# Kernel optimization log

Hardware: AMD Instinct MI355X
Metric: run time of the kernel (lower is better)

The kernel has to match this reference:

```python
import jax, jax.numpy as jnp
import numpy as np

B, C, H, W = 16, 96, 64, 64
N = H * W
BN = B * N
K = 16  # neighbors per node
E = BN * K
C_OUT = 96


def setup_inputs() -> dict:
    key = jax.random.key(0)
    k1, k2, k3, k4 = jax.random.split(key, 4)
    x = jax.random.normal(k1, (B, C, H, W), dtype=jnp.float32)
    # KNN-style edge list over flat node ids (node = b*N + n):
    # every node appears K times as a target (row 0), random sources (row 1).
    dst = jnp.repeat(jnp.arange(BN, dtype=jnp.int64), K)
    src = jax.random.randint(k2, (E,), 0, BN, dtype=jnp.int64)
    edge_index = jnp.stack([dst, src], axis=0)
    Wc = jax.random.normal(k3, (C_OUT, 2 * C), dtype=jnp.float32) * 0.05
    bc = jax.random.normal(k4, (C_OUT,), dtype=jnp.float32) * 0.05
    return {"x": x, "edge_index": edge_index, "Wc": Wc, "bc": bc}


def reference(x, edge_index, Wc, bc):
    b, c, h, w = x.shape
    n = h * w
    # Flatten to node features [B*N, C] with node id = b*N + n
    feats = x.reshape(b, c, n).transpose(0, 2, 1).reshape(b * n, c)
    # Max-relative aggregation: gather, subtract, scatter-max over targets
    diff = feats[edge_index[1]] - feats[edge_index[0]]        # [E, C]
    agg = jax.ops.segment_max(diff, edge_index[0], num_segments=b * n)  # [BN, C]
    x_j = agg.reshape(b, n, c).transpose(0, 2, 1)             # [B, C, N]
    x_n = x.reshape(b, c, n)                                   # [B, C, N]
    # Interleaved channel concat: (x_0, xj_0, x_1, xj_1, ...) -> [B, 2C, N]
    cat = jnp.stack([x_n, x_j], axis=2).reshape(b, 2 * c, n)
    # BasicConv: 1x1 conv (GEMM over channels) + bias + ReLU
    out = jnp.einsum('oc,bcn->bon', Wc, cat) + bc[None, :, None]
    out = jax.nn.relu(out)
    return out.reshape(b, -1, h, w)
```

## Files before the change

### kernel.cpp

```cpp
#include <hip/hip_runtime.h>

#define B_   16
#define C_   96
#define N_   4096
#define BN_  65536
#define K_   16
#define E_   (BN_ * K_)

typedef __attribute__((ext_vector_type(8))) short bf16x8;
typedef __attribute__((ext_vector_type(4))) float f32x4;

union FragU { uint32_t u[4]; bf16x8 v; };

__device__ __forceinline__ uint32_t pack2_bf16(float a, float b) {
    uint32_t ua = __builtin_bit_cast(uint32_t, a);
    uint32_t ub = __builtin_bit_cast(uint32_t, b);
    ua = (ua + 0x7fffu + ((ua >> 16) & 1u)) >> 16;
    ub = (ub + 0x7fffu + ((ub >> 16) & 1u)) >> 16;
    return (ua & 0xffffu) | (ub << 16);
}
__device__ __forceinline__ float lo16f(uint32_t u) {
    return __builtin_bit_cast(float, u << 16);
}
__device__ __forceinline__ float hi16f(uint32_t u) {
    return __builtin_bit_cast(float, u & 0xffff0000u);
}

__global__ __launch_bounds__(256) void transpose_k(const float* __restrict__ x,
                                                   ushort* __restrict__ feats_bf) {
    __shared__ float tile[32][65];
    int b  = blockIdx.z;
    int c0 = blockIdx.y * 32;
    int n0 = blockIdx.x * 64;
    const float* xp = x + (size_t)b * C_ * N_;
    for (int t = threadIdx.x; t < 32 * 64; t += 256) {
        int c = t >> 6, n = t & 63;
        tile[c][n] = xp[(size_t)(c0 + c) * N_ + n0 + n];
    }
    __syncthreads();
    ushort* fp = feats_bf + ((size_t)b * N_ + n0) * C_ + c0;
    for (int t = threadIdx.x; t < 64 * 16; t += 256) {
        int n = t >> 4, cq = t & 15;
        uint32_t p = pack2_bf16(tile[2 * cq][n], tile[2 * cq + 1][n]);
        *(uint32_t*)(fp + (size_t)n * C_ + 2 * cq) = p;
    }
}

__global__ __launch_bounds__(256) void gather_max_k(const ushort* __restrict__ feats,
                                                    const int* __restrict__ src,
                                                    ushort* __restrict__ agg_bf,
                                                    const float* __restrict__ Wc,
                                                    ushort* __restrict__ Wp) {
    int tid = threadIdx.x;
    if (blockIdx.x >= 2048) {
        int t = (blockIdx.x - 2048) * 256 + tid;
        if (t >= 36 * 64) return;
        int fid = t >> 6, l = t & 63;
        int ks = fid / 6, to = fid % 6;
        int o = to * 16 + (l & 15), g = l >> 4;
        uint32_t packed[4];
#pragma unroll
        for (int h = 0; h < 4; h++) {
            int e0 = 2 * h, e1 = 2 * h + 1;
            int k0 = ks * 32 + 4 * g + (e0 & 3) + 16 * (e0 >> 2);
            int k1 = ks * 32 + 4 * g + (e1 & 3) + 16 * (e1 >> 2);
            int ko0 = (k0 < 96) ? 2 * k0 : 2 * (k0 - 96) + 1;
            int ko1 = (k1 < 96) ? 2 * k1 : 2 * (k1 - 96) + 1;
            packed[h] = pack2_bf16(Wc[(size_t)o * 192 + ko0],
                                   Wc[(size_t)o * 192 + ko1]);
        }
        ((uint4*)Wp)[t] = make_uint4(packed[0], packed[1], packed[2], packed[3]);
        return;
    }

    int ln  = tid >> 3;
    int r   = tid & 7;
    size_t i = (size_t)blockIdx.x * 32 + ln;
    const int* s = src + i * K_;

    float m[12];
#pragma unroll
    for (int j = 0; j < 12; j++) m[j] = -3.0e38f;

#pragma unroll
    for (int q = 0; q < 4; q++) {
        int4 iv = ((const int4*)s)[q];
        int ids[4] = {iv.x, iv.y, iv.z, iv.w};
#pragma unroll
        for (int kk = 0; kk < 4; kk++) {
            const uint2* row = (const uint2*)(feats + (size_t)ids[kk] * C_);
#pragma unroll
            for (int j = 0; j < 3; j++) {
                uint2 v = row[r + 8 * j];
                m[4 * j + 0] = fmaxf(m[4 * j + 0], lo16f(v.x));
                m[4 * j + 1] = fmaxf(m[4 * j + 1], hi16f(v.x));
                m[4 * j + 2] = fmaxf(m[4 * j + 2], lo16f(v.y));
                m[4 * j + 3] = fmaxf(m[4 * j + 3], hi16f(v.y));
            }
        }
    }

    const uint2* own = (const uint2*)(feats + i * (size_t)C_);
    ushort* ap = agg_bf + i * (size_t)C_;
#pragma unroll
    for (int j = 0; j < 3; j++) {
        uint2 o = own[r + 8 * j];
        uint2 p;
        p.x = pack2_bf16(m[4 * j + 0] - lo16f(o.x), m[4 * j + 1] - hi16f(o.x));
        p.y = pack2_bf16(m[4 * j + 2] - lo16f(o.y), m[4 * j + 3] - hi16f(o.y));
        *(uint2*)(ap + (size_t)(r + 8 * j) * 4) = p;
    }
}

__global__ __launch_bounds__(512) void conv_mfma_k(const ushort* __restrict__ feats_bf,
                                                   const ushort* __restrict__ agg_bf,
                                                   const ushort* __restrict__ Wp,
                                                   const float* __restrict__ bc,
                                                   float* __restrict__ out) {
    __shared__ ushort A_lds[128 * 200];
    int tid = threadIdx.x;
    int w = tid >> 6, l = tid & 63;
    int blk = blockIdx.x;
    int b = blk >> 5;
    int n0 = (blk & 31) << 7;

    float bcr[6];
#pragma unroll
    for (int to = 0; to < 6; to++) bcr[to] = bc[to * 16 + (l & 15)];

    const ushort* fb = feats_bf + ((size_t)b * N_ + n0) * C_;
    const ushort* ab = agg_bf + ((size_t)b * N_ + n0) * C_;
#pragma unroll
    for (int i = 0; i < 6; i++) {
        int tau = i * 512 + tid;
        int n = tau / 24;
        int p = tau - n * 24;
        const ushort* srcp = (p < 12) ? (fb + (size_t)n * C_ + 8 * p)
                                      : (ab + (size_t)n * C_ + 8 * (p - 12));
        uint4 u = *(const uint4*)srcp;
        if (n & 1) { uint32_t t0 = u.x, t1 = u.y; u.x = u.z; u.y = u.w; u.z = t0; u.w = t1; }
        int slot = p ^ ((n >> 1) & 7);
        *(uint4*)&A_lds[n * 200 + slot * 8] = u;
    }
    __syncthreads();

    f32x4 acc[6];
#pragma unroll
    for (int to = 0; to < 6; to++) acc[to] = (f32x4){0.f, 0.f, 0.f, 0.f};

    const uint4* wp4 = (const uint4*)Wp;
    int g = l >> 4;
    int m = (l & 15) << 2;
    int nrow = w * 16 + (l & 15);
    int abase = nrow * 200;

#pragma unroll
    for (int ks = 0; ks < 6; ks++) {
        FragU bfrag[6];
#pragma unroll
        for (int to = 0; to < 6; to++) {
            uint4 u = wp4[(ks * 6 + to) * 64 + l];
            bfrag[to].u[0] = u.x; bfrag[to].u[1] = u.y;
            bfrag[to].u[2] = u.z; bfrag[to].u[3] = u.w;
        }
        int k1 = ks * 32 + 4 * g;
        uint2 lo = *(const uint2*)&A_lds[abase + (k1 ^ m)];
        uint2 hi = *(const uint2*)&A_lds[abase + ((k1 + 16) ^ m)];
        FragU afrag;
        afrag.u[0] = lo.x; afrag.u[1] = lo.y;
        afrag.u[2] = hi.x; afrag.u[3] = hi.y;
#pragma unroll
        for (int to = 0; to < 6; to++)
            acc[to] = __builtin_amdgcn_mfma_f32_16x16x32_bf16(
                afrag.v, bfrag[to].v, acc[to], 0, 0, 0);
    }

    int nl = n0 + w * 16 + ((l >> 4) << 2);
#pragma unroll
    for (int to = 0; to < 6; to++) {
        int o = to * 16 + (l & 15);
        float4 v;
        v.x = fmaxf(acc[to][0] + bcr[to], 0.0f);
        v.y = fmaxf(acc[to][1] + bcr[to], 0.0f);
        v.z = fmaxf(acc[to][2] + bcr[to], 0.0f);
        v.w = fmaxf(acc[to][3] + bcr[to], 0.0f);
        *(float4*)(out + ((size_t)b * C_ + o) * N_ + nl) = v;
    }
}

extern "C" void kernel_launch(void* const* d_in, const int* in_sizes, int n_in,
                              void* d_out, int out_size, void* d_ws, size_t ws_size,
                              hipStream_t stream) {
    const float* x   = (const float*)d_in[0];
    const int*   ei  = (const int*)d_in[1];
    const float* Wc  = (const float*)d_in[2];
    const float* bc  = (const float*)d_in[3];
    float* out = (float*)d_out;

    const int* src = ei + E_;

    ushort* feats_bf = (ushort*)d_ws;
    ushort* agg_bf   = (ushort*)((char*)d_ws + (size_t)BN_ * C_ * 2);
    ushort* Wp       = (ushort*)((char*)d_ws + (size_t)BN_ * C_ * 4);

    dim3 gA(N_ / 64, C_ / 32, B_);
    transpose_k<<<gA, 256, 0, stream>>>(x, feats_bf);

    gather_max_k<<<2057, 256, 0, stream>>>(feats_bf, src, agg_bf, Wc, Wp);

    conv_mfma_k<<<B_ * (N_ / 128), 512, 0, stream>>>(feats_bf, agg_bf, Wp, bc, out);
}
```

Before: 57.01 us.

## Fuse gather-max aggregation into conv kernel and weight packing into transpose

Moves the neighbor gather/max-relative aggregation into the MFMA conv kernel, which writes the aggregated bf16 features straight into the shared-memory A tile instead of round-tripping them through a global agg buffer. Weight packing moves into the transpose kernel, cutting the pipeline from three launches to two. This removes the global write and re-read of agg and one launch, but the conv kernel now has only 512 blocks doing latency-bound random gathers (two nodes per thread), so less parallelism is available to hide gather latency.

```diff
diff --git a/kernel.cpp b/kernel.cpp
--- a/kernel.cpp
+++ b/kernel.cpp
@@ -26,34 +26,13 @@
     return __builtin_bit_cast(float, u & 0xffff0000u);
 }
 
-__global__ __launch_bounds__(256) void transpose_k(const float* __restrict__ x,
-                                                   ushort* __restrict__ feats_bf) {
-    __shared__ float tile[32][65];
-    int b  = blockIdx.z;
-    int c0 = blockIdx.y * 32;
-    int n0 = blockIdx.x * 64;
-    const float* xp = x + (size_t)b * C_ * N_;
-    for (int t = threadIdx.x; t < 32 * 64; t += 256) {
-        int c = t >> 6, n = t & 63;
-        tile[c][n] = xp[(size_t)(c0 + c) * N_ + n0 + n];
-    }
-    __syncthreads();
-    ushort* fp = feats_bf + ((size_t)b * N_ + n0) * C_ + c0;
-    for (int t = threadIdx.x; t < 64 * 16; t += 256) {
-        int n = t >> 4, cq = t & 15;
-        uint32_t p = pack2_bf16(tile[2 * cq][n], tile[2 * cq + 1][n]);
-        *(uint32_t*)(fp + (size_t)n * C_ + 2 * cq) = p;
-    }
-}
-
-__global__ __launch_bounds__(256) void gather_max_k(const ushort* __restrict__ feats,
-                                                    const int* __restrict__ src,
-                                                    ushort* __restrict__ agg_bf,
-                                                    const float* __restrict__ Wc,
-                                                    ushort* __restrict__ Wp) {
-    int tid = threadIdx.x;
-    if (blockIdx.x >= 2048) {
-        int t = (blockIdx.x - 2048) * 256 + tid;
+__global__ __launch_bounds__(256) void transpose_pack_k(const float* __restrict__ x,
+                                                        ushort* __restrict__ feats_bf,
+                                                        const float* __restrict__ Wc,
+                                                        ushort* __restrict__ Wp) {
+    int blk = blockIdx.x;
+    if (blk >= 3072) {
+        int t = (blk - 3072) * 256 + threadIdx.x;
         if (t >= 36 * 64) return;
         int fid = t >> 6, l = t & 63;
         int ks = fid / 6, to = fid % 6;
@@ -72,51 +51,30 @@
         ((uint4*)Wp)[t] = make_uint4(packed[0], packed[1], packed[2], packed[3]);
         return;
     }
-
-    int ln  = tid >> 3;
-    int r   = tid & 7;
-    size_t i = (size_t)blockIdx.x * 32 + ln;
-    const int* s = src + i * K_;
-
-    float m[12];
-#pragma unroll
-    for (int j = 0; j < 12; j++) m[j] = -3.0e38f;
-
-#pragma unroll
-    for (int q = 0; q < 4; q++) {
-        int4 iv = ((const int4*)s)[q];
-        int ids[4] = {iv.x, iv.y, iv.z, iv.w};
-#pragma unroll
-        for (int kk = 0; kk < 4; kk++) {
-            const uint2* row = (const uint2*)(feats + (size_t)ids[kk] * C_);
-#pragma unroll
-            for (int j = 0; j < 3; j++) {
-                uint2 v = row[r + 8 * j];
-                m[4 * j + 0] = fmaxf(m[4 * j + 0], lo16f(v.x));
-                m[4 * j + 1] = fmaxf(m[4 * j + 1], hi16f(v.x));
-                m[4 * j + 2] = fmaxf(m[4 * j + 2], lo16f(v.y));
-                m[4 * j + 3] = fmaxf(m[4 * j + 3], hi16f(v.y));
-            }
-        }
-    }
-
-    const uint2* own = (const uint2*)(feats + i * (size_t)C_);
-    ushort* ap = agg_bf + i * (size_t)C_;
-#pragma unroll
-    for (int j = 0; j < 3; j++) {
-        uint2 o = own[r + 8 * j];
-        uint2 p;
-        p.x = pack2_bf16(m[4 * j + 0] - lo16f(o.x), m[4 * j + 1] - hi16f(o.x));
-        p.y = pack2_bf16(m[4 * j + 2] - lo16f(o.y), m[4 * j + 3] - hi16f(o.y));
-        *(uint2*)(ap + (size_t)(r + 8 * j) * 4) = p;
-    }
-}
-
-__global__ __launch_bounds__(512) void conv_mfma_k(const ushort* __restrict__ feats_bf,
-                                                   const ushort* __restrict__ agg_bf,
-                                                   const ushort* __restrict__ Wp,
-                                                   const float* __restrict__ bc,
-                                                   float* __restrict__ out) {
+    __shared__ float tile[32][65];
+    int b   = blk / 192;
+    int rem = blk - b * 192;
+    int c0  = (rem >> 6) * 32;
+    int n0  = (rem & 63) * 64;
+    const float* xp = x + (size_t)b * C_ * N_;
+    for (int t = threadIdx.x; t < 32 * 64; t += 256) {
+        int c = t >> 6, n = t & 63;
+        tile[c][n] = xp[(size_t)(c0 + c) * N_ + n0 + n];
+    }
+    __syncthreads();
+    ushort* fp = feats_bf + ((size_t)b * N_ + n0) * C_ + c0;
+    for (int t = threadIdx.x; t < 64 * 16; t += 256) {
+        int n = t >> 4, cq = t & 15;
+        uint32_t p = pack2_bf16(tile[2 * cq][n], tile[2 * cq + 1][n]);
+        *(uint32_t*)(fp + (size_t)n * C_ + 2 * cq) = p;
+    }
+}
+
+__global__ __launch_bounds__(512) void gconv_k(const ushort* __restrict__ feats,
+                                               const int* __restrict__ src,
+                                               const ushort* __restrict__ Wp,
+                                               const float* __restrict__ bc,
+                                               float* __restrict__ out) {
     __shared__ ushort A_lds[128 * 200];
     int tid = threadIdx.x;
     int w = tid >> 6, l = tid & 63;
@@ -124,25 +82,64 @@
     int b = blk >> 5;
     int n0 = (blk & 31) << 7;
 
-    float bcr[6];
-#pragma unroll
-    for (int to = 0; to < 6; to++) bcr[to] = bc[to * 16 + (l & 15)];
-
-    const ushort* fb = feats_bf + ((size_t)b * N_ + n0) * C_;
-    const ushort* ab = agg_bf + ((size_t)b * N_ + n0) * C_;
-#pragma unroll
-    for (int i = 0; i < 6; i++) {
+    const ushort* fb = feats + ((size_t)b * N_ + n0) * C_;
+#pragma unroll
+    for (int i = 0; i < 3; i++) {
         int tau = i * 512 + tid;
-        int n = tau / 24;
-        int p = tau - n * 24;
-        const ushort* srcp = (p < 12) ? (fb + (size_t)n * C_ + 8 * p)
-                                      : (ab + (size_t)n * C_ + 8 * (p - 12));
-        uint4 u = *(const uint4*)srcp;
+        int n = tau / 12;
+        int p = tau - n * 12;
+        uint4 u = *(const uint4*)(fb + (size_t)n * C_ + 8 * p);
         if (n & 1) { uint32_t t0 = u.x, t1 = u.y; u.x = u.z; u.y = u.w; u.z = t0; u.w = t1; }
         int slot = p ^ ((n >> 1) & 7);
         *(uint4*)&A_lds[n * 200 + slot * 8] = u;
     }
+
+#pragma unroll
+    for (int s = 0; s < 2; s++) {
+        int ln = s * 64 + (tid >> 3);
+        int r  = tid & 7;
+        size_t i = (size_t)b * N_ + n0 + ln;
+        const int* sp = src + i * K_;
+
+        float m[12];
+#pragma unroll
+        for (int j = 0; j < 12; j++) m[j] = -3.0e38f;
+
+#pragma unroll
+        for (int q = 0; q < 4; q++) {
+            int4 iv = ((const int4*)sp)[q];
+            int ids[4] = {iv.x, iv.y, iv.z, iv.w};
+#pragma unroll
+            for (int kk = 0; kk < 4; kk++) {
+                const uint2* row = (const uint2*)(feats + (size_t)ids[kk] * C_);
+#pragma unroll
+                for (int j = 0; j < 3; j++) {
+                    uint2 v = row[r + 8 * j];
+                    m[4 * j + 0] = fmaxf(m[4 * j + 0], lo16f(v.x));
+                    m[4 * j + 1] = fmaxf(m[4 * j + 1], hi16f(v.x));
+                    m[4 * j + 2] = fmaxf(m[4 * j + 2], lo16f(v.y));
+                    m[4 * j + 3] = fmaxf(m[4 * j + 3], hi16f(v.y));
+                }
+            }
+        }
+
+        const uint2* own = (const uint2*)(feats + i * (size_t)C_);
+#pragma unroll
+        for (int j = 0; j < 3; j++) {
+            uint2 o = own[r + 8 * j];
+            uint2 p;
+            p.x = pack2_bf16(m[4 * j + 0] - lo16f(o.x), m[4 * j + 1] - hi16f(o.x));
+            p.y = pack2_bf16(m[4 * j + 2] - lo16f(o.y), m[4 * j + 3] - hi16f(o.y));
+            int qa = r + 8 * j;
+            int idx = ln * 200 + ((96 + 4 * qa) ^ ((ln & 15) << 2));
+            *(uint2*)&A_lds[idx] = p;
+        }
+    }
     __syncthreads();
+
+    float bcr[6];
+#pragma unroll
+    for (int to = 0; to < 6; to++) bcr[to] = bc[to * 16 + (l & 15)];
 
     f32x4 acc[6];
 #pragma unroll
@@ -150,9 +147,8 @@
 
     const uint4* wp4 = (const uint4*)Wp;
     int g = l >> 4;
-    int m = (l & 15) << 2;
-    int nrow = w * 16 + (l & 15);
-    int abase = nrow * 200;
+    int msk = (l & 15) << 2;
+    int abase = (w * 16 + (l & 15)) * 200;
 
 #pragma unroll
     for (int ks = 0; ks < 6; ks++) {
@@ -164,8 +160,8 @@
             bfrag[to].u[2] = u.z; bfrag[to].u[3] = u.w;
         }
         int k1 = ks * 32 + 4 * g;
-        uint2 lo = *(const uint2*)&A_lds[abase + (k1 ^ m)];
-        uint2 hi = *(const uint2*)&A_lds[abase + ((k1 + 16) ^ m)];
+        uint2 lo = *(const uint2*)&A_lds[abase + (k1 ^ msk)];
+        uint2 hi = *(const uint2*)&A_lds[abase + ((k1 + 16) ^ msk)];
         FragU afrag;
         afrag.u[0] = lo.x; afrag.u[1] = lo.y;
         afrag.u[2] = hi.x; afrag.u[3] = hi.y;
@@ -200,13 +196,9 @@
     const int* src = ei + E_;
 
     ushort* feats_bf = (ushort*)d_ws;
-    ushort* agg_bf   = (ushort*)((char*)d_ws + (size_t)BN_ * C_ * 2);
-    ushort* Wp       = (ushort*)((char*)d_ws + (size_t)BN_ * C_ * 4);
-
-    dim3 gA(N_ / 64, C_ / 32, B_);
-    transpose_k<<<gA, 256, 0, stream>>>(x, feats_bf);
-
-    gather_max_k<<<2057, 256, 0, stream>>>(feats_bf, src, agg_bf, Wc, Wp);
-
-    conv_mfma_k<<<B_ * (N_ / 128), 512, 0, stream>>>(feats_bf, agg_bf, Wp, bc, out);
-}
+    ushort* Wp       = (ushort*)((char*)d_ws + (size_t)BN_ * C_ * 2);
+
+    transpose_pack_k<<<3081, 256, 0, stream>>>(x, feats_bf, Wc, Wp);
+
+    gconv_k<<<B_ * (N_ / 128), 512, 0, stream>>>(feats_bf, src, Wp, bc, out);
+}
```

Measured after the change: 53.05 us. 6.9% less time.
